# Kernel tuning notes

Measured on AMD Instinct MI355X. Metric: run time of the kernel, lower is better.

Reference implementation:

```python
import jax, jax.numpy as jnp
import numpy as np

N_STATE = 1024
N_HEAD = 16


def setup_inputs() -> dict:
    key = jax.random.key(0)
    ks = jax.random.split(key, 8)
    B, C, H, W = 4, N_STATE, 1, 1500
    s = C ** -0.5
    return {
        "x": jax.random.normal(ks[0], (B, C, H, W), dtype=jnp.float32),
        "Wq": jax.random.normal(ks[1], (C, C), dtype=jnp.float32) * s,
        "bq": jnp.zeros((C,), dtype=jnp.float32),
        "Wk": jax.random.normal(ks[2], (C, C), dtype=jnp.float32) * s,
        "Wv": jax.random.normal(ks[3], (C, C), dtype=jnp.float32) * s,
        "bv": jnp.zeros((C,), dtype=jnp.float32),
        "Wo": jax.random.normal(ks[4], (C, C), dtype=jnp.float32) * s,
        "bo": jnp.zeros((C,), dtype=jnp.float32),
    }


def reference(x, Wq, bq, Wk, Wv, bv, Wo, bo):
    B, C, H, W = x.shape
    nh = N_HEAD
    d = C // nh
    scale = d ** -0.5

    def conv1x1(w, b=None):
        y = jnp.einsum('bchw,oc->bohw', x, w)  # 1x1 conv == per-pixel matmul
        return y if b is None else y + b[None, :, None, None]

    # [B, nh, d, H, W] per-head layout (channel split matches torch .split)
    q = conv1x1(Wq, bq).reshape(B, nh, d, H, W)
    k = conv1x1(Wk).reshape(B, nh, d, H, W)
    v = conv1x1(Wv, bv).reshape(B, nh, d, H, W)

    # attention along width axis, independently per height row and head
    scores = jnp.einsum('bndhq,bndhk->bnhqk', q, k) * scale  # [B,nh,H,Wq,Wk]
    attn = jax.nn.softmax(scores, axis=-1)                   # softmax over keys
    o = jnp.einsum('bnhqk,bndhk->bndhq', attn, v).reshape(B, C, H, W)
    return jnp.einsum('bchw,oc->bohw', o, Wo) + bo[None, :, None, None]
```

## Files before the change

### kernel.cpp

```cpp
#include <hip/hip_runtime.h>
#include <stdint.h>


typedef unsigned short u16;
typedef __bf16 bf16x8 __attribute__((ext_vector_type(8)));
typedef float  f32x4  __attribute__((ext_vector_type(4)));
typedef unsigned int __attribute__((address_space(1))) as1_uint;
typedef unsigned int __attribute__((address_space(3))) as3_uint;

__device__ __forceinline__ u16 f2bf(float f) {
    unsigned u = __float_as_uint(f);
    u += 0x7fffu + ((u >> 16) & 1u);
    return (u16)(u >> 16);
}

__device__ __forceinline__ f32x4 fzero4() { f32x4 z = {0.f, 0.f, 0.f, 0.f}; return z; }

__device__ __forceinline__ void gld16(void* lds, const void* g) {
    __builtin_amdgcn_global_load_lds((const as1_uint*)g, (as3_uint*)lds, 16, 0, 0);
}

__device__ __forceinline__ int permw(int w) {
    return (w & ~31) | ((w & 12) << 1) | ((w & 16) >> 2) | (w & 3);
}

__global__ void prep_k(const float* __restrict__ wq, const float* __restrict__ wk,
                       const float* __restrict__ wv, const float* __restrict__ wo,
                       u16* __restrict__ wb, const float* __restrict__ x,
                       u16* __restrict__ xb) {
    __shared__ float tile[64][65];
    const int bid = blockIdx.x;
    if (bid < 4096) {
        unsigned idx = bid * 256u + threadIdx.x;
        unsigned m = idx >> 18, r = idx & 0x3ffffu;
        const float* s = (m == 0) ? wq : (m == 1) ? wk : (m == 2) ? wv : wo;
        float4 v = ((const float4*)s)[r];
        uint2 o;
        o.x = (unsigned)f2bf(v.x) | ((unsigned)f2bf(v.y) << 16);
        o.y = (unsigned)f2bf(v.z) | ((unsigned)f2bf(v.w) << 16);
        ((uint2*)(wb + (m << 20)))[r] = o;
    } else {
        int bid2 = bid - 4096;
        const int xw = bid2 % 24, yc = (bid2 / 24) & 15, b = bid2 / 384;
        const int w0 = xw * 64, c0 = yc * 64;
        const int tw = threadIdx.x & 63, t4 = threadIdx.x >> 6;
#pragma unroll
        for (int i = 0; i < 16; i++) {
            int c = i * 4 + t4, w = w0 + tw;
            tile[c][tw] = (w < 1500) ? x[((b << 10) + c0 + c) * 1500 + w] : 0.f;
        }
        __syncthreads();
#pragma unroll
        for (int i = 0; i < 16; i++) {
            int wl = i * 4 + t4, w = w0 + wl;
            if (w < 1500) xb[((b * 1500 + w) << 10) + c0 + tw] = f2bf(tile[tw][wl]);
        }
    }
}

__device__ __forceinline__ void stage_db(const u16* __restrict__ A, int arow0, int amax,
                                         const u16* __restrict__ Bm, int brow0, int bmax,
                                         int k0, unsigned char* lds, int buf) {
    const int t = threadIdx.x;
    unsigned char* ab = lds + (buf << 14);
    unsigned char* bb = lds + 32768 + (buf << 14);
#pragma unroll
    for (int i = 0; i < 4; i++) {
        int xo = (i * 256 + t) << 4;
        int row = xo >> 7, seg = (xo >> 4) & 7;
        int sseg = seg ^ (row & 7);
        int ar = arow0 + row; if (ar > amax) ar = amax;
        int br = brow0 + row; if (br > bmax) br = bmax;
        gld16(ab + xo, A  + ((long)ar << 10) + k0 + sseg * 8);
        gld16(bb + xo, Bm + ((long)br << 10) + k0 + sseg * 8);
    }
}

__device__ __forceinline__ void gemm_core_db(const u16* __restrict__ A, int arow0, int amax,
                                             const u16* __restrict__ Bm, int brow0, int bmax,
                                             f32x4 (&acc)[4][4], unsigned char* lds) {
    const int t = threadIdx.x, l15 = t & 15, lg = (t >> 4) & 3;
    const int wv = t >> 6, wm = wv >> 1, wn = wv & 1;
    const int l7 = l15 & 7;
#pragma unroll
    for (int im = 0; im < 4; im++)
#pragma unroll
        for (int in = 0; in < 4; in++) acc[im][in] = fzero4();

    stage_db(A, arow0, amax, Bm, brow0, bmax, 0, lds, 0);
    __syncthreads();

    for (int kt = 0; kt < 16; kt++) {
        const int cur = kt & 1;
        if (kt < 15)
            stage_db(A, arow0, amax, Bm, brow0, bmax, (kt + 1) << 6, lds, cur ^ 1);
        const unsigned char* ab = lds + (cur << 14);
        const unsigned char* bb = lds + 32768 + (cur << 14);
#pragma unroll
        for (int ks = 0; ks < 2; ks++) {
            bf16x8 af[4], bfr[4];
#pragma unroll
            for (int im = 0; im < 4; im++) {
                int row = wm * 64 + im * 16 + l15;
                af[im] = *(const bf16x8*)(ab + (row << 7) + (((ks * 4 + lg) ^ l7) << 4));
            }
#pragma unroll
            for (int in = 0; in < 4; in++) {
                int row = wn * 64 + in * 16 + l15;
                bfr[in] = *(const bf16x8*)(bb + (row << 7) + (((ks * 4 + lg) ^ l7) << 4));
            }
#pragma unroll
            for (int im = 0; im < 4; im++)
#pragma unroll
                for (int in = 0; in < 4; in++)
                    acc[im][in] = __builtin_amdgcn_mfma_f32_16x16x32_bf16(af[im], bfr[in], acc[im][in], 0, 0, 0);
        }
        if (kt < 15) __syncthreads();
    }
}

__global__ __launch_bounds__(256) void qkv_k(const u16* __restrict__ xb, const u16* __restrict__ wb,
                                             const float* __restrict__ bq, const float* __restrict__ bv,
                                             u16* __restrict__ Q, u16* __restrict__ K,
                                             u16* __restrict__ Vt) {
    __shared__ __attribute__((aligned(16))) unsigned char lds[65536];
    const int p = blockIdx.x;
    const int bid = (p & 7) * 142 + (p >> 3);
    const int t = threadIdx.x, l15 = t & 15, lg = (t >> 4) & 3;
    const int wv = t >> 6, wm = wv >> 1, wn = wv & 1;
    f32x4 acc[4][4];

    if (bid < 752) {
        const int z = bid / 376, rem = bid % 376;
        const int xt = rem % 47, yt = rem / 47;
        gemm_core_db(xb, xt * 128, 5999, wb + (z << 20), yt * 128, 1023, acc, lds);
        const int m0 = xt * 128 + wm * 64, n0 = yt * 128 + wn * 64;
        u16* dst = z ? K : Q;
        const float* bias = z ? nullptr : bq;
#pragma unroll
        for (int im = 0; im < 4; im++) {
#pragma unroll
            for (int r = 0; r < 4; r++) {
                int tok = m0 + im * 16 + lg * 4 + r;
                if (tok < 6000) {
                    int b = tok / 1500, w = tok - b * 1500;
#pragma unroll
                    for (int in = 0; in < 4; in++) {
                        int o = n0 + in * 16 + l15;
                        float v = acc[im][in][r] + (bias ? bias[o] : 0.f);
                        dst[((((b << 4) + (o >> 6)) * 1500 + w) << 6) + (o & 63)] = f2bf(v);
                    }
                }
            }
        }
    } else {
        const int rem = bid - 752;
        const int xt = rem & 7, rest = rem >> 3;
        const int yt = rest % 12, b = rest / 12;
        gemm_core_db(wb + (2u << 20), xt * 128, 1023, xb + b * 1500 * 1024, yt * 128, 1499, acc, lds);
        const int m0 = xt * 128 + wm * 64, n0 = yt * 128 + wn * 64;
#pragma unroll
        for (int im = 0; im < 4; im++) {
#pragma unroll
            for (int r = 0; r < 4; r++) {
                int o = m0 + im * 16 + lg * 4 + r;
                float bi = bv[o];
#pragma unroll
                for (int in = 0; in < 4; in++) {
                    int w = n0 + in * 16 + l15;
                    if (w < 1504) {
                        u16 val = (w < 1500) ? f2bf(acc[im][in][r] + bi) : (u16)0;
                        Vt[((b << 10) + o) * 1504 + permw(w)] = val;
                    }
                }
            }
        }
    }
}

__global__ __launch_bounds__(256) void gemm_out_k(const u16* __restrict__ Ow, const u16* __restrict__ wb,
                                                  const float* __restrict__ bo, float* __restrict__ out) {
    __shared__ __attribute__((aligned(16))) unsigned char lds[65536];
    const int p = blockIdx.x;
    const int lb = (p & 7) * 47 + (p >> 3);
    const int xt = lb & 7, nt = lb >> 3;
    f32x4 acc[4][4];
    gemm_core_db(wb + (3u << 20), xt * 128, 1023, Ow, nt * 128, 5999, acc, lds);
    const int t = threadIdx.x, l15 = t & 15, lg = (t >> 4) & 3;
    const int wv = t >> 6, wm = wv >> 1, wn = wv & 1;
    const int m0 = xt * 128 + wm * 64;
    const int n0 = nt * 128 + wn * 64;
#pragma unroll
    for (int im = 0; im < 4; im++) {
#pragma unroll
        for (int r = 0; r < 4; r++) {
            int o = m0 + im * 16 + lg * 4 + r;
            float bi = bo[o];
#pragma unroll
            for (int in = 0; in < 4; in++) {
                int tok = n0 + in * 16 + l15;
                if (tok < 6000) {
                    int b = tok / 1500, w = tok - b * 1500;
                    out[(long)((b << 10) + o) * 1500 + w] = acc[im][in][r] + bi;
                }
            }
        }
    }
}

__global__ __launch_bounds__(512) void attn_k(const u16* __restrict__ Q, const u16* __restrict__ K,
                                              const u16* __restrict__ Vt, u16* __restrict__ O) {
    __shared__ __attribute__((aligned(16))) unsigned char lds[32768];

    const int qt = blockIdx.x, bh = blockIdx.y;
    const int b = bh >> 4, h = bh & 15;
    const int t = threadIdx.x, wv = t >> 6, l15 = t & 15, g = (t >> 4) & 3;
    const int sk7 = l15 & 7;

    int q_a = qt * 128 + wv * 16 + l15; if (q_a > 1499) q_a = 1499;
    const u16* qrow = Q + (((long)bh * 1500 + q_a) << 6);
    bf16x8 qb0 = *(const bf16x8*)(qrow + (g << 3));
    bf16x8 qb1 = *(const bf16x8*)(qrow + 32 + (g << 3));

    const u16* Kbh = K + (((long)bh * 1500) << 6);
    const u16* Vtb = Vt + (long)((b << 10) + (h << 6)) * 1504;

    const int srow = t >> 3;
    const int ssw  = ((t & 7) ^ (srow & 7)) << 3;
    unsigned char* kdst = lds + (t << 4);
    unsigned char* vdst = lds + 16384 + (t << 4);

    f32x4 o_acc[4];
#pragma unroll
    for (int nf = 0; nf < 4; nf++) o_acc[nf] = fzero4();
    float m_run = -1e30f, l_part = 0.f;
    const float SC = 0.18033688011112042f;

    gld16(kdst, Kbh + ((long)srow << 6) + ssw);
    gld16(vdst, Vtb + (long)srow * 1504 + ssw);
    __syncthreads();

    for (int tile = 0; tile < 24; ++tile) {
        const int cur = tile & 1;
        if (tile < 23) {
            int kv0 = (tile + 1) << 6;
            int kg = kv0 + srow; if (kg > 1499) kg = 1499;
            gld16(kdst + ((cur ^ 1) << 13), Kbh + ((long)kg << 6) + ssw);
            int vc = kv0 + ssw; if (vc > 1496) vc = 1496;
            gld16(vdst + ((cur ^ 1) << 13), Vtb + (long)srow * 1504 + vc);
        }
        const unsigned char* Kl = lds + (cur << 13);
        const unsigned char* Vl = lds + 16384 + (cur << 13);

        f32x4 s[4];
        __builtin_amdgcn_s_setprio(1);
#pragma unroll
        for (int kt = 0; kt < 4; kt++) {
            const unsigned char* kp = Kl + ((kt * 16 + l15) << 7);
            bf16x8 ka0 = *(const bf16x8*)(kp + ((g ^ sk7) << 4));
            bf16x8 ka1 = *(const bf16x8*)(kp + (((g + 4) ^ sk7) << 4));
            f32x4 z = fzero4();
            z = __builtin_amdgcn_mfma_f32_16x16x32_bf16(ka0, qb0, z, 0, 0, 0);
            z = __builtin_amdgcn_mfma_f32_16x16x32_bf16(ka1, qb1, z, 0, 0, 0);
            s[kt] = z;
        }
        __builtin_amdgcn_s_setprio(0);
        if (tile == 23) {
#pragma unroll
            for (int kt = 0; kt < 4; kt++)
#pragma unroll
                for (int r = 0; r < 4; r++)
                    if (kt * 16 + g * 4 + r >= 28) s[kt][r] = -1e30f;
        }

        float m1 = fmaxf(fmaxf(s[0][0], s[0][1]), s[0][2]);
        float m2 = fmaxf(fmaxf(s[0][3], s[1][0]), s[1][1]);
        float m3 = fmaxf(fmaxf(s[1][2], s[1][3]), s[2][0]);
        float m4 = fmaxf(fmaxf(s[2][1], s[2][2]), s[2][3]);
        float m5 = fmaxf(fmaxf(s[3][0], s[3][1]), s[3][2]);
        float mx = fmaxf(fmaxf(fmaxf(m1, m2), m3), fmaxf(fmaxf(m4, m5), s[3][3]));
        mx = fmaxf(mx, __shfl_xor(mx, 16));
        mx = fmaxf(mx, __shfl_xor(mx, 32));

        if (!__all(mx <= m_run + 44.f)) {
            float mnew = fmaxf(m_run, mx);
            float sc = exp2f((m_run - mnew) * SC);
            l_part *= sc;
#pragma unroll
            for (int r = 0; r < 4; r++) {
                float sco = __shfl(sc, g * 4 + r);
#pragma unroll
                for (int nf = 0; nf < 4; nf++) o_acc[nf][r] *= sco;
            }
            m_run = mnew;
        }

        const float msc = m_run * SC;
        float pv[4][4];
        float psum = 0.f;
#pragma unroll
        for (int kt = 0; kt < 4; kt++) {
#pragma unroll
            for (int r = 0; r < 4; r++) {
                float p2 = exp2f(fmaf(s[kt][r], SC, -msc));
                pv[kt][r] = p2;
                psum += p2;
            }
        }
        l_part += psum;

        bf16x8 pa0, pa1;
#pragma unroll
        for (int j = 0; j < 8; j++) {
            pa0[j] = (__bf16)pv[j >> 2][j & 3];
            pa1[j] = (__bf16)pv[2 + (j >> 2)][j & 3];
        }

        __builtin_amdgcn_s_setprio(1);
#pragma unroll
        for (int nf = 0; nf < 4; nf++) {
            const unsigned char* vp = Vl + ((nf * 16 + l15) << 7);
            bf16x8 vb0 = *(const bf16x8*)(vp + ((g ^ sk7) << 4));
            bf16x8 vb1 = *(const bf16x8*)(vp + (((4 + g) ^ sk7) << 4));
            o_acc[nf] = __builtin_amdgcn_mfma_f32_16x16x32_bf16(pa0, vb0, o_acc[nf], 0, 0, 0);
            o_acc[nf] = __builtin_amdgcn_mfma_f32_16x16x32_bf16(pa1, vb1, o_acc[nf], 0, 0, 0);
        }
        __builtin_amdgcn_s_setprio(0);
        __syncthreads();
    }

    l_part += __shfl_xor(l_part, 16);
    l_part += __shfl_xor(l_part, 32);
    float inv = 1.f / l_part;
#pragma unroll
    for (int r = 0; r < 4; r++) {
        float invr = __shfl(inv, g * 4 + r);
        int q = qt * 128 + wv * 16 + g * 4 + r;
        if (q < 1500) {
            u16* dst = O + ((long)(b * 1500 + q) << 10) + (h << 6);
#pragma unroll
            for (int nf = 0; nf < 4; nf++)
                dst[nf * 16 + l15] = f2bf(o_acc[nf][r] * invr);
        }
    }
}

extern "C" void kernel_launch(void* const* d_in, const int* in_sizes, int n_in,
                              void* d_out, int out_size, void* d_ws, size_t ws_size,
                              hipStream_t stream) {
    const float* x  = (const float*)d_in[0];
    const float* Wq = (const float*)d_in[1];
    const float* bq = (const float*)d_in[2];
    const float* Wk = (const float*)d_in[3];
    const float* Wv = (const float*)d_in[4];
    const float* bv = (const float*)d_in[5];
    const float* Wo = (const float*)d_in[6];
    const float* bo = (const float*)d_in[7];
    float* out = (float*)d_out;

    const size_t NEED = 57573376;
    if (ws_size < NEED) return;

    unsigned char* ws = (unsigned char*)d_ws;
    u16* xb = (u16*)(ws);
    u16* wb = (u16*)(ws + 12288000);
    u16* Qw = (u16*)(ws + 20676608);
    u16* Kw = (u16*)(ws + 32964608);
    u16* Vt = (u16*)(ws + 45252608);

    prep_k<<<dim3(5632), dim3(256), 0, stream>>>(Wq, Wk, Wv, Wo, wb, x, xb);
    qkv_k<<<dim3(1136), dim3(256), 0, stream>>>(xb, wb, bq, bv, Qw, Kw, Vt);
    attn_k<<<dim3(12, 64), dim3(512), 0, stream>>>(Qw, Kw, Vt, xb );
    gemm_out_k<<<dim3(376), dim3(256), 0, stream>>>(xb, wb, bo, out);
}
```

Baseline: 190.1 us.

## Switch GEMMs to 256x256 tiles with 512 threads and fused Q/K projection

Replaces the 128x128, 256-thread GEMM core with a 256x256 tile over 8 waves. Each k-step is now 32 wide with a 4-segment LDS swizzle, which raises arithmetic intensity per staged byte. The Q and K projections are merged into one GEMM over a concatenated 2048-row weight, and the V projection now tiles across all tokens. The Vt padding columns are zeroed in a new prep block, and attention and output launches get XCD-aware block remapping. The larger tiles cut the grid to 288 and 96 blocks, which risks poor CU occupancy and tail imbalance on a 256-CU part.

```diff
diff --git a/kernel.cpp b/kernel.cpp
--- a/kernel.cpp
+++ b/kernel.cpp
@@ -27,7 +27,7 @@
 __global__ void prep_k(const float* __restrict__ wq, const float* __restrict__ wk,
                        const float* __restrict__ wv, const float* __restrict__ wo,
                        u16* __restrict__ wb, const float* __restrict__ x,
-                       u16* __restrict__ xb) {
+                       u16* __restrict__ xb, u16* __restrict__ Vt) {
     __shared__ float tile[64][65];
     const int bid = blockIdx.x;
     if (bid < 4096) {
@@ -39,7 +39,7 @@
         o.x = (unsigned)f2bf(v.x) | ((unsigned)f2bf(v.y) << 16);
         o.y = (unsigned)f2bf(v.z) | ((unsigned)f2bf(v.w) << 16);
         ((uint2*)(wb + (m << 20)))[r] = o;
-    } else {
+    } else if (bid < 5632) {
         int bid2 = bid - 4096;
         const int xw = bid2 % 24, yc = (bid2 / 24) & 15, b = bid2 / 384;
         const int w0 = xw * 64, c0 = yc * 64;
@@ -55,20 +55,28 @@
             int wl = i * 4 + t4, w = w0 + wl;
             if (w < 1500) xb[((b * 1500 + w) << 10) + c0 + tw] = f2bf(tile[tw][wl]);
         }
-    }
-}
-
-__device__ __forceinline__ void stage_db(const u16* __restrict__ A, int arow0, int amax,
-                                         const u16* __restrict__ Bm, int brow0, int bmax,
-                                         int k0, unsigned char* lds, int buf) {
+    } else {
+        const int t = threadIdx.x;
+        uint2 z; z.x = 0u; z.y = 0u;
+#pragma unroll
+        for (int i = 0; i < 16; i++) {
+            int idx = i * 256 + t;
+            *(uint2*)(Vt + (long)idx * 1504 + 1500) = z;
+        }
+    }
+}
+
+__device__ __forceinline__ void stage32(const u16* __restrict__ A, int arow0, int amax,
+                                        const u16* __restrict__ Bm, int brow0, int bmax,
+                                        int k0, unsigned char* lds, int buf) {
     const int t = threadIdx.x;
     unsigned char* ab = lds + (buf << 14);
     unsigned char* bb = lds + 32768 + (buf << 14);
 #pragma unroll
-    for (int i = 0; i < 4; i++) {
-        int xo = (i * 256 + t) << 4;
-        int row = xo >> 7, seg = (xo >> 4) & 7;
-        int sseg = seg ^ (row & 7);
+    for (int i = 0; i < 2; i++) {
+        int xo = (i * 512 + t) << 4;
+        int row = xo >> 6, seg = (xo >> 4) & 3;
+        int sseg = seg ^ ((row >> 1) & 3);
         int ar = arow0 + row; if (ar > amax) ar = amax;
         int br = brow0 + row; if (br > bmax) br = bmax;
         gld16(ab + xo, A  + ((long)ar << 10) + k0 + sseg * 8);
@@ -76,69 +84,60 @@
     }
 }
 
-__device__ __forceinline__ void gemm_core_db(const u16* __restrict__ A, int arow0, int amax,
+__device__ __forceinline__ void gemm_core256(const u16* __restrict__ A, int arow0, int amax,
                                              const u16* __restrict__ Bm, int brow0, int bmax,
-                                             f32x4 (&acc)[4][4], unsigned char* lds) {
+                                             f32x4 (&acc)[8][4], unsigned char* lds) {
     const int t = threadIdx.x, l15 = t & 15, lg = (t >> 4) & 3;
-    const int wv = t >> 6, wm = wv >> 1, wn = wv & 1;
-    const int l7 = l15 & 7;
-#pragma unroll
-    for (int im = 0; im < 4; im++)
+    const int wv = t >> 6, wm = wv >> 2, wn = wv & 3;
+#pragma unroll
+    for (int im = 0; im < 8; im++)
 #pragma unroll
         for (int in = 0; in < 4; in++) acc[im][in] = fzero4();
 
-    stage_db(A, arow0, amax, Bm, brow0, bmax, 0, lds, 0);
+    stage32(A, arow0, amax, Bm, brow0, bmax, 0, lds, 0);
     __syncthreads();
 
-    for (int kt = 0; kt < 16; kt++) {
+    for (int kt = 0; kt < 32; kt++) {
         const int cur = kt & 1;
-        if (kt < 15)
-            stage_db(A, arow0, amax, Bm, brow0, bmax, (kt + 1) << 6, lds, cur ^ 1);
+        if (kt < 31)
+            stage32(A, arow0, amax, Bm, brow0, bmax, (kt + 1) << 5, lds, cur ^ 1);
         const unsigned char* ab = lds + (cur << 14);
         const unsigned char* bb = lds + 32768 + (cur << 14);
-#pragma unroll
-        for (int ks = 0; ks < 2; ks++) {
-            bf16x8 af[4], bfr[4];
-#pragma unroll
-            for (int im = 0; im < 4; im++) {
-                int row = wm * 64 + im * 16 + l15;
-                af[im] = *(const bf16x8*)(ab + (row << 7) + (((ks * 4 + lg) ^ l7) << 4));
-            }
-#pragma unroll
-            for (int in = 0; in < 4; in++) {
-                int row = wn * 64 + in * 16 + l15;
-                bfr[in] = *(const bf16x8*)(bb + (row << 7) + (((ks * 4 + lg) ^ l7) << 4));
-            }
-#pragma unroll
-            for (int im = 0; im < 4; im++)
-#pragma unroll
-                for (int in = 0; in < 4; in++)
-                    acc[im][in] = __builtin_amdgcn_mfma_f32_16x16x32_bf16(af[im], bfr[in], acc[im][in], 0, 0, 0);
-        }
-        if (kt < 15) __syncthreads();
-    }
-}
-
-__global__ __launch_bounds__(256) void qkv_k(const u16* __restrict__ xb, const u16* __restrict__ wb,
-                                             const float* __restrict__ bq, const float* __restrict__ bv,
-                                             u16* __restrict__ Q, u16* __restrict__ K,
-                                             u16* __restrict__ Vt) {
+        bf16x8 bfr[4];
+#pragma unroll
+        for (int in = 0; in < 4; in++) {
+            int row = wn * 64 + in * 16 + l15;
+            bfr[in] = *(const bf16x8*)(bb + (row << 6) + ((lg ^ ((row >> 1) & 3)) << 4));
+        }
+#pragma unroll
+        for (int im = 0; im < 8; im++) {
+            int row = wm * 128 + im * 16 + l15;
+            bf16x8 af = *(const bf16x8*)(ab + (row << 6) + ((lg ^ ((row >> 1) & 3)) << 4));
+#pragma unroll
+            for (int in = 0; in < 4; in++)
+                acc[im][in] = __builtin_amdgcn_mfma_f32_16x16x32_bf16(af, bfr[in], acc[im][in], 0, 0, 0);
+        }
+        if (kt < 31) __syncthreads();
+    }
+}
+
+__global__ __launch_bounds__(512, 2) void qkv_k(const u16* __restrict__ xb, const u16* __restrict__ wb,
+                                                const float* __restrict__ bq, const float* __restrict__ bv,
+                                                u16* __restrict__ Q, u16* __restrict__ K,
+                                                u16* __restrict__ Vt) {
     __shared__ __attribute__((aligned(16))) unsigned char lds[65536];
     const int p = blockIdx.x;
-    const int bid = (p & 7) * 142 + (p >> 3);
+    const int lb = (p & 7) * 36 + (p >> 3);
     const int t = threadIdx.x, l15 = t & 15, lg = (t >> 4) & 3;
-    const int wv = t >> 6, wm = wv >> 1, wn = wv & 1;
-    f32x4 acc[4][4];
-
-    if (bid < 752) {
-        const int z = bid / 376, rem = bid % 376;
-        const int xt = rem % 47, yt = rem / 47;
-        gemm_core_db(xb, xt * 128, 5999, wb + (z << 20), yt * 128, 1023, acc, lds);
-        const int m0 = xt * 128 + wm * 64, n0 = yt * 128 + wn * 64;
-        u16* dst = z ? K : Q;
-        const float* bias = z ? nullptr : bq;
-#pragma unroll
-        for (int im = 0; im < 4; im++) {
+    const int wv = t >> 6, wm = wv >> 2, wn = wv & 3;
+    f32x4 acc[8][4];
+
+    if (lb < 192) {
+        const int xt = lb % 24, yt = lb / 24;
+        gemm_core256(xb, xt * 256, 5999, wb, yt * 256, 2047, acc, lds);
+        const int m0 = xt * 256 + wm * 128, n0 = yt * 256 + wn * 64;
+#pragma unroll
+        for (int im = 0; im < 8; im++) {
 #pragma unroll
             for (int r = 0; r < 4; r++) {
                 int tok = m0 + im * 16 + lg * 4 + r;
@@ -146,31 +145,32 @@
                     int b = tok / 1500, w = tok - b * 1500;
 #pragma unroll
                     for (int in = 0; in < 4; in++) {
-                        int o = n0 + in * 16 + l15;
-                        float v = acc[im][in][r] + (bias ? bias[o] : 0.f);
+                        int oc = n0 + in * 16 + l15;
+                        float v = acc[im][in][r] + (oc < 1024 ? bq[oc] : 0.f);
+                        u16* dst = (oc < 1024) ? Q : K;
+                        int o = oc & 1023;
                         dst[((((b << 4) + (o >> 6)) * 1500 + w) << 6) + (o & 63)] = f2bf(v);
                     }
                 }
             }
         }
     } else {
-        const int rem = bid - 752;
-        const int xt = rem & 7, rest = rem >> 3;
-        const int yt = rest % 12, b = rest / 12;
-        gemm_core_db(wb + (2u << 20), xt * 128, 1023, xb + b * 1500 * 1024, yt * 128, 1499, acc, lds);
-        const int m0 = xt * 128 + wm * 64, n0 = yt * 128 + wn * 64;
-#pragma unroll
-        for (int im = 0; im < 4; im++) {
+        const int r2 = lb - 192;
+        const int xt = r2 & 3, yt = r2 >> 2;
+        gemm_core256(wb + (2u << 20), xt * 256, 1023, xb, yt * 256, 5999, acc, lds);
+        const int m0 = xt * 256 + wm * 128, n0 = yt * 256 + wn * 64;
+#pragma unroll
+        for (int im = 0; im < 8; im++) {
 #pragma unroll
             for (int r = 0; r < 4; r++) {
                 int o = m0 + im * 16 + lg * 4 + r;
                 float bi = bv[o];
 #pragma unroll
                 for (int in = 0; in < 4; in++) {
-                    int w = n0 + in * 16 + l15;
-                    if (w < 1504) {
-                        u16 val = (w < 1500) ? f2bf(acc[im][in][r] + bi) : (u16)0;
-                        Vt[((b << 10) + o) * 1504 + permw(w)] = val;
+                    int tok = n0 + in * 16 + l15;
+                    if (tok < 6000) {
+                        int b = tok / 1500, w = tok - b * 1500;
+                        Vt[((b << 10) + o) * 1504 + permw(w)] = f2bf(acc[im][in][r] + bi);
                     }
                 }
             }
@@ -178,20 +178,19 @@
     }
 }
 
-__global__ __launch_bounds__(256) void gemm_out_k(const u16* __restrict__ Ow, const u16* __restrict__ wb,
-                                                  const float* __restrict__ bo, float* __restrict__ out) {
+__global__ __launch_bounds__(512, 2) void gemm_out_k(const u16* __restrict__ Ow, const u16* __restrict__ wb,
+                                                     const float* __restrict__ bo, float* __restrict__ out) {
     __shared__ __attribute__((aligned(16))) unsigned char lds[65536];
     const int p = blockIdx.x;
-    const int lb = (p & 7) * 47 + (p >> 3);
-    const int xt = lb & 7, nt = lb >> 3;
-    f32x4 acc[4][4];
-    gemm_core_db(wb + (3u << 20), xt * 128, 1023, Ow, nt * 128, 5999, acc, lds);
+    const int lb = (p & 7) * 12 + (p >> 3);
+    const int xt = lb & 3, nt = lb >> 2;
     const int t = threadIdx.x, l15 = t & 15, lg = (t >> 4) & 3;
-    const int wv = t >> 6, wm = wv >> 1, wn = wv & 1;
-    const int m0 = xt * 128 + wm * 64;
-    const int n0 = nt * 128 + wn * 64;
-#pragma unroll
-    for (int im = 0; im < 4; im++) {
+    const int wv = t >> 6, wm = wv >> 2, wn = wv & 3;
+    f32x4 acc[8][4];
+    gemm_core256(wb + (3u << 20), xt * 256, 1023, Ow, nt * 256, 5999, acc, lds);
+    const int m0 = xt * 256 + wm * 128, n0 = nt * 256 + wn * 64;
+#pragma unroll
+    for (int im = 0; im < 8; im++) {
 #pragma unroll
         for (int r = 0; r < 4; r++) {
             int o = m0 + im * 16 + lg * 4 + r;
@@ -212,7 +211,9 @@
                                               const u16* __restrict__ Vt, u16* __restrict__ O) {
     __shared__ __attribute__((aligned(16))) unsigned char lds[32768];
 
-    const int qt = blockIdx.x, bh = blockIdx.y;
+    const int p = blockIdx.x;
+    const int lb = (p & 7) * 96 + (p >> 3);
+    const int qt = lb % 12, bh = lb / 12;
     const int b = bh >> 4, h = bh & 15;
     const int t = threadIdx.x, wv = t >> 6, l15 = t & 15, g = (t >> 4) & 3;
     const int sk7 = l15 & 7;
@@ -368,8 +369,8 @@
     u16* Kw = (u16*)(ws + 32964608);
     u16* Vt = (u16*)(ws + 45252608);
 
-    prep_k<<<dim3(5632), dim3(256), 0, stream>>>(Wq, Wk, Wv, Wo, wb, x, xb);
-    qkv_k<<<dim3(1136), dim3(256), 0, stream>>>(xb, wb, bq, bv, Qw, Kw, Vt);
-    attn_k<<<dim3(12, 64), dim3(512), 0, stream>>>(Qw, Kw, Vt, xb );
-    gemm_out_k<<<dim3(376), dim3(256), 0, stream>>>(xb, wb, bo, out);
-}
+    prep_k<<<dim3(5633), dim3(256), 0, stream>>>(Wq, Wk, Wv, Wo, wb, x, xb, Vt);
+    qkv_k<<<dim3(288), dim3(512), 0, stream>>>(xb, wb, bq, bv, Qw, Kw, Vt);
+    attn_k<<<dim3(768), dim3(512), 0, stream>>>(Qw, Kw, Vt, xb );
+    gemm_out_k<<<dim3(96), dim3(512), 0, stream>>>(xb, wb, bo, out);
+}
```

After: 224.2 us. 1.18x slower.

## Halve GEMM K-tile to 32 for higher occupancy, remap attention grid, prezero V padding

Applied to the files above, without the earlier changes.

The GEMM core now stages K-slices of 32 instead of 64, which halves LDS use to 32KB per block. A new XOR swizzle fits the 64-byte rows, and launch bounds ask for 5 blocks per CU so more waves can hide latency. The cost is twice as many k-iterations and barriers. Attention blocks move to a 1D grid with an XCD-aware remap so neighbouring query tiles of one head share an L2 slice, and the Vt padding columns are zeroed once in prep_k instead of inside the V GEMM epilogue.

```diff
diff --git a/kernel.cpp b/kernel.cpp
--- a/kernel.cpp
+++ b/kernel.cpp
@@ -27,7 +27,7 @@
 __global__ void prep_k(const float* __restrict__ wq, const float* __restrict__ wk,
                        const float* __restrict__ wv, const float* __restrict__ wo,
                        u16* __restrict__ wb, const float* __restrict__ x,
-                       u16* __restrict__ xb) {
+                       u16* __restrict__ xb, u16* __restrict__ Vt) {
     __shared__ float tile[64][65];
     const int bid = blockIdx.x;
     if (bid < 4096) {
@@ -39,7 +39,7 @@
         o.x = (unsigned)f2bf(v.x) | ((unsigned)f2bf(v.y) << 16);
         o.y = (unsigned)f2bf(v.z) | ((unsigned)f2bf(v.w) << 16);
         ((uint2*)(wb + (m << 20)))[r] = o;
-    } else {
+    } else if (bid < 5632) {
         int bid2 = bid - 4096;
         const int xw = bid2 % 24, yc = (bid2 / 24) & 15, b = bid2 / 384;
         const int w0 = xw * 64, c0 = yc * 64;
@@ -55,20 +55,28 @@
             int wl = i * 4 + t4, w = w0 + wl;
             if (w < 1500) xb[((b * 1500 + w) << 10) + c0 + tw] = f2bf(tile[tw][wl]);
         }
-    }
-}
-
-__device__ __forceinline__ void stage_db(const u16* __restrict__ A, int arow0, int amax,
-                                         const u16* __restrict__ Bm, int brow0, int bmax,
-                                         int k0, unsigned char* lds, int buf) {
+    } else {
+        const int t = threadIdx.x;
+        uint2 z; z.x = 0u; z.y = 0u;
+#pragma unroll
+        for (int i = 0; i < 16; i++) {
+            int idx = i * 256 + t;
+            *(uint2*)(Vt + (long)idx * 1504 + 1500) = z;
+        }
+    }
+}
+
+__device__ __forceinline__ void stage32(const u16* __restrict__ A, int arow0, int amax,
+                                        const u16* __restrict__ Bm, int brow0, int bmax,
+                                        int k0, unsigned char* lds, int buf) {
     const int t = threadIdx.x;
-    unsigned char* ab = lds + (buf << 14);
-    unsigned char* bb = lds + 32768 + (buf << 14);
-#pragma unroll
-    for (int i = 0; i < 4; i++) {
+    unsigned char* ab = lds + (buf << 13);
+    unsigned char* bb = lds + 16384 + (buf << 13);
+#pragma unroll
+    for (int i = 0; i < 2; i++) {
         int xo = (i * 256 + t) << 4;
-        int row = xo >> 7, seg = (xo >> 4) & 7;
-        int sseg = seg ^ (row & 7);
+        int row = xo >> 6, seg = (xo >> 4) & 3;
+        int sseg = seg ^ ((row >> 1) & 3);
         int ar = arow0 + row; if (ar > amax) ar = amax;
         int br = brow0 + row; if (br > bmax) br = bmax;
         gld16(ab + xo, A  + ((long)ar << 10) + k0 + sseg * 8);
@@ -76,54 +84,50 @@
     }
 }
 
-__device__ __forceinline__ void gemm_core_db(const u16* __restrict__ A, int arow0, int amax,
+__device__ __forceinline__ void gemm_core128(const u16* __restrict__ A, int arow0, int amax,
                                              const u16* __restrict__ Bm, int brow0, int bmax,
                                              f32x4 (&acc)[4][4], unsigned char* lds) {
     const int t = threadIdx.x, l15 = t & 15, lg = (t >> 4) & 3;
     const int wv = t >> 6, wm = wv >> 1, wn = wv & 1;
-    const int l7 = l15 & 7;
 #pragma unroll
     for (int im = 0; im < 4; im++)
 #pragma unroll
         for (int in = 0; in < 4; in++) acc[im][in] = fzero4();
 
-    stage_db(A, arow0, amax, Bm, brow0, bmax, 0, lds, 0);
+    stage32(A, arow0, amax, Bm, brow0, bmax, 0, lds, 0);
     __syncthreads();
 
-    for (int kt = 0; kt < 16; kt++) {
+    for (int kt = 0; kt < 32; kt++) {
         const int cur = kt & 1;
-        if (kt < 15)
-            stage_db(A, arow0, amax, Bm, brow0, bmax, (kt + 1) << 6, lds, cur ^ 1);
-        const unsigned char* ab = lds + (cur << 14);
-        const unsigned char* bb = lds + 32768 + (cur << 14);
-#pragma unroll
-        for (int ks = 0; ks < 2; ks++) {
-            bf16x8 af[4], bfr[4];
-#pragma unroll
-            for (int im = 0; im < 4; im++) {
-                int row = wm * 64 + im * 16 + l15;
-                af[im] = *(const bf16x8*)(ab + (row << 7) + (((ks * 4 + lg) ^ l7) << 4));
-            }
-#pragma unroll
-            for (int in = 0; in < 4; in++) {
-                int row = wn * 64 + in * 16 + l15;
-                bfr[in] = *(const bf16x8*)(bb + (row << 7) + (((ks * 4 + lg) ^ l7) << 4));
-            }
-#pragma unroll
-            for (int im = 0; im < 4; im++)
-#pragma unroll
-                for (int in = 0; in < 4; in++)
-                    acc[im][in] = __builtin_amdgcn_mfma_f32_16x16x32_bf16(af[im], bfr[in], acc[im][in], 0, 0, 0);
-        }
-        if (kt < 15) __syncthreads();
-    }
-}
-
-__global__ __launch_bounds__(256) void qkv_k(const u16* __restrict__ xb, const u16* __restrict__ wb,
-                                             const float* __restrict__ bq, const float* __restrict__ bv,
-                                             u16* __restrict__ Q, u16* __restrict__ K,
-                                             u16* __restrict__ Vt) {
-    __shared__ __attribute__((aligned(16))) unsigned char lds[65536];
+        if (kt < 31)
+            stage32(A, arow0, amax, Bm, brow0, bmax, (kt + 1) << 5, lds, cur ^ 1);
+        const unsigned char* ab = lds + (cur << 13);
+        const unsigned char* bb = lds + 16384 + (cur << 13);
+        bf16x8 af[4], bfr[4];
+#pragma unroll
+        for (int im = 0; im < 4; im++) {
+            int row = wm * 64 + im * 16 + l15;
+            af[im] = *(const bf16x8*)(ab + (row << 6) + ((lg ^ ((row >> 1) & 3)) << 4));
+        }
+#pragma unroll
+        for (int in = 0; in < 4; in++) {
+            int row = wn * 64 + in * 16 + l15;
+            bfr[in] = *(const bf16x8*)(bb + (row << 6) + ((lg ^ ((row >> 1) & 3)) << 4));
+        }
+#pragma unroll
+        for (int im = 0; im < 4; im++)
+#pragma unroll
+            for (int in = 0; in < 4; in++)
+                acc[im][in] = __builtin_amdgcn_mfma_f32_16x16x32_bf16(af[im], bfr[in], acc[im][in], 0, 0, 0);
+        if (kt < 31) __syncthreads();
+    }
+}
+
+__global__ __launch_bounds__(256, 5) void qkv_k(const u16* __restrict__ xb, const u16* __restrict__ wb,
+                                                const float* __restrict__ bq, const float* __restrict__ bv,
+                                                u16* __restrict__ Q, u16* __restrict__ K,
+                                                u16* __restrict__ Vt) {
+    __shared__ __attribute__((aligned(16))) unsigned char lds[32768];
     const int p = blockIdx.x;
     const int bid = (p & 7) * 142 + (p >> 3);
     const int t = threadIdx.x, l15 = t & 15, lg = (t >> 4) & 3;
@@ -133,7 +137,7 @@
     if (bid < 752) {
         const int z = bid / 376, rem = bid % 376;
         const int xt = rem % 47, yt = rem / 47;
-        gemm_core_db(xb, xt * 128, 5999, wb + (z << 20), yt * 128, 1023, acc, lds);
+        gemm_core128(xb, xt * 128, 5999, wb + (z << 20), yt * 128, 1023, acc, lds);
         const int m0 = xt * 128 + wm * 64, n0 = yt * 128 + wn * 64;
         u16* dst = z ? K : Q;
         const float* bias = z ? nullptr : bq;
@@ -157,7 +161,7 @@
         const int rem = bid - 752;
         const int xt = rem & 7, rest = rem >> 3;
         const int yt = rest % 12, b = rest / 12;
-        gemm_core_db(wb + (2u << 20), xt * 128, 1023, xb + b * 1500 * 1024, yt * 128, 1499, acc, lds);
+        gemm_core128(wb + (2u << 20), xt * 128, 1023, xb + b * 1500 * 1024, yt * 128, 1499, acc, lds);
         const int m0 = xt * 128 + wm * 64, n0 = yt * 128 + wn * 64;
 #pragma unroll
         for (int im = 0; im < 4; im++) {
@@ -168,24 +172,22 @@
 #pragma unroll
                 for (int in = 0; in < 4; in++) {
                     int w = n0 + in * 16 + l15;
-                    if (w < 1504) {
-                        u16 val = (w < 1500) ? f2bf(acc[im][in][r] + bi) : (u16)0;
-                        Vt[((b << 10) + o) * 1504 + permw(w)] = val;
-                    }
+                    if (w < 1500)
+                        Vt[((b << 10) + o) * 1504 + permw(w)] = f2bf(acc[im][in][r] + bi);
                 }
             }
         }
     }
 }
 
-__global__ __launch_bounds__(256) void gemm_out_k(const u16* __restrict__ Ow, const u16* __restrict__ wb,
-                                                  const float* __restrict__ bo, float* __restrict__ out) {
-    __shared__ __attribute__((aligned(16))) unsigned char lds[65536];
+__global__ __launch_bounds__(256, 5) void gemm_out_k(const u16* __restrict__ Ow, const u16* __restrict__ wb,
+                                                     const float* __restrict__ bo, float* __restrict__ out) {
+    __shared__ __attribute__((aligned(16))) unsigned char lds[32768];
     const int p = blockIdx.x;
     const int lb = (p & 7) * 47 + (p >> 3);
     const int xt = lb & 7, nt = lb >> 3;
     f32x4 acc[4][4];
-    gemm_core_db(wb + (3u << 20), xt * 128, 1023, Ow, nt * 128, 5999, acc, lds);
+    gemm_core128(wb + (3u << 20), xt * 128, 1023, Ow, nt * 128, 5999, acc, lds);
     const int t = threadIdx.x, l15 = t & 15, lg = (t >> 4) & 3;
     const int wv = t >> 6, wm = wv >> 1, wn = wv & 1;
     const int m0 = xt * 128 + wm * 64;
@@ -212,7 +214,9 @@
                                               const u16* __restrict__ Vt, u16* __restrict__ O) {
     __shared__ __attribute__((aligned(16))) unsigned char lds[32768];
 
-    const int qt = blockIdx.x, bh = blockIdx.y;
+    const int p = blockIdx.x;
+    const int lb = (p & 7) * 96 + (p >> 3);
+    const int qt = lb % 12, bh = lb / 12;
     const int b = bh >> 4, h = bh & 15;
     const int t = threadIdx.x, wv = t >> 6, l15 = t & 15, g = (t >> 4) & 3;
     const int sk7 = l15 & 7;
@@ -368,8 +372,8 @@
     u16* Kw = (u16*)(ws + 32964608);
     u16* Vt = (u16*)(ws + 45252608);
 
-    prep_k<<<dim3(5632), dim3(256), 0, stream>>>(Wq, Wk, Wv, Wo, wb, x, xb);
+    prep_k<<<dim3(5633), dim3(256), 0, stream>>>(Wq, Wk, Wv, Wo, wb, x, xb, Vt);
     qkv_k<<<dim3(1136), dim3(256), 0, stream>>>(xb, wb, bq, bv, Qw, Kw, Vt);
-    attn_k<<<dim3(12, 64), dim3(512), 0, stream>>>(Qw, Kw, Vt, xb );
+    attn_k<<<dim3(768), dim3(512), 0, stream>>>(Qw, Kw, Vt, xb );
     gemm_out_k<<<dim3(376), dim3(256), 0, stream>>>(xb, wb, bo, out);
 }
```

Result: slower. 204.3 us (+7.4%).
